# Performance work log

Measured on AMD Instinct MI355X. Metric: run time of the kernel, lower is better.

## Reference

```python
import jax, jax.numpy as jnp
import numpy as np

N, E, D, H, ED = 10000, 160000, 512, 256, 16
EPS = 1e-5  # BatchNorm1d eps


def _cgconv(x, src, dst, edge_attr, Wf, bf, Ws, bs, gamma, beta, mean, var):
    # PyG CGConv: z = [x_i, x_j, e_ij]; m = sigmoid(lin_f(z)) * softplus(lin_s(z));
    # aggr='add' at target i; batch_norm (eval mode, running stats) then residual.
    z = jnp.concatenate([x[dst], x[src], edge_attr], axis=1)  # [E, 2D+ED]
    m = jax.nn.sigmoid(z @ Wf + bf) * jax.nn.softplus(z @ Ws + bs)  # [E, D]
    aggr = jax.ops.segment_sum(m, dst, num_segments=x.shape[0])  # [N, D]
    bn = (aggr - mean) * jax.lax.rsqrt(var + EPS) * gamma + beta
    return x + bn


def _gcnconv(x, src, dst, W, b):
    # PyG GCNConv with add_self_loops=True, normalize=True:
    n = x.shape[0]
    deg = jax.ops.segment_sum(jnp.ones((src.shape[0],), x.dtype), dst, num_segments=n) + 1.0
    dinv = jax.lax.rsqrt(deg)  # [N]
    h = x @ W  # [N, out]
    out = jax.ops.segment_sum((dinv[src] * dinv[dst])[:, None] * h[src], dst, num_segments=n)
    out = out + (dinv * dinv)[:, None] * h  # self-loop contribution
    return out + b


def _forward(x, edge_attr, goal_feat,
             cg1_Wf, cg1_bf, cg1_Ws, cg1_bs, cg1_gamma, cg1_beta, cg1_mean, cg1_var,
             cg2_Wf, cg2_bf, cg2_Ws, cg2_bs, cg2_gamma, cg2_beta, cg2_mean, cg2_var,
             gcn3_W, gcn3_b, gcn4_W, gcn4_b, d1_W, d1_b, d2_W, d2_b, src, dst):
    # dropout layers are identity in eval mode (self.training=False)
    x = jax.nn.relu(_cgconv(x, src, dst, edge_attr, cg1_Wf, cg1_bf, cg1_Ws, cg1_bs,
                            cg1_gamma, cg1_beta, cg1_mean, cg1_var))
    x = jax.nn.relu(_cgconv(x, src, dst, edge_attr, cg2_Wf, cg2_bf, cg2_Ws, cg2_bs,
                            cg2_gamma, cg2_beta, cg2_mean, cg2_var))
    x = jax.nn.relu(_gcnconv(x, src, dst, gcn3_W, gcn3_b))
    x = jax.nn.relu(_gcnconv(x, src, dst, gcn4_W, gcn4_b))
    g = jnp.broadcast_to(goal_feat, (x.shape[0], goal_feat.shape[1]))  # repeat(num_nodes, 1)
    h = jax.nn.relu(jnp.concatenate([x, g], axis=1) @ d1_W + d1_b)
    return h @ d2_W + d2_b  # [N, 1]


def setup_inputs() -> dict:
    ks = jax.random.split(jax.random.key(0), 12)
    w = lambda k, s: jax.random.normal(k, s, dtype=jnp.float32) * 0.02
    Z = 2 * D + ED
    return {
        "x": jax.random.normal(ks[0], (N, D), jnp.float32),
        "edge_attr": jax.random.normal(ks[1], (E, ED), jnp.float32),
        "goal_feat": jax.random.normal(ks[2], (1, D), jnp.float32),
        "cg1_Wf": w(ks[3], (Z, D)), "cg1_bf": jnp.zeros((D,), jnp.float32),
        "cg1_Ws": w(ks[4], (Z, D)), "cg1_bs": jnp.zeros((D,), jnp.float32),
        "cg1_gamma": jnp.ones((D,), jnp.float32), "cg1_beta": jnp.zeros((D,), jnp.float32),
        "cg1_mean": jnp.zeros((D,), jnp.float32), "cg1_var": jnp.ones((D,), jnp.float32),
        "cg2_Wf": w(ks[5], (Z, D)), "cg2_bf": jnp.zeros((D,), jnp.float32),
        "cg2_Ws": w(ks[6], (Z, D)), "cg2_bs": jnp.zeros((D,), jnp.float32),
        "cg2_gamma": jnp.ones((D,), jnp.float32), "cg2_beta": jnp.zeros((D,), jnp.float32),
        "cg2_mean": jnp.zeros((D,), jnp.float32), "cg2_var": jnp.ones((D,), jnp.float32),
        "gcn3_W": w(ks[7], (D, H)), "gcn3_b": jnp.zeros((H,), jnp.float32),
        "gcn4_W": w(ks[8], (H, H)), "gcn4_b": jnp.zeros((H,), jnp.float32),
        "d1_W": w(ks[9], (H + D, D)), "d1_b": jnp.zeros((D,), jnp.float32),
        "d2_W": w(ks[10], (D, 1)), "d2_b": jnp.zeros((1,), jnp.float32),
        "edge_index": jax.random.randint(ks[11], (2, E), 0, N, dtype=jnp.int32),
        "batch": jnp.zeros((N,), jnp.int32),
    }


def reference(x, edge_attr, goal_feat,
              cg1_Wf, cg1_bf, cg1_Ws, cg1_bs, cg1_gamma, cg1_beta, cg1_mean, cg1_var,
              cg2_Wf, cg2_bf, cg2_Ws, cg2_bs, cg2_gamma, cg2_beta, cg2_mean, cg2_var,
              gcn3_W, gcn3_b, gcn4_W, gcn4_b, d1_W, d1_b, d2_W, d2_b,
              edge_index, batch):
    src, dst = edge_index[0], edge_index[1]
    return _forward(x, edge_attr, goal_feat,
                    cg1_Wf, cg1_bf, cg1_Ws, cg1_bs, cg1_gamma, cg1_beta, cg1_mean, cg1_var,
                    cg2_Wf, cg2_bf, cg2_Ws, cg2_bs, cg2_gamma, cg2_beta, cg2_mean, cg2_var,
                    gcn3_W, gcn3_b, gcn4_W, gcn4_b, d1_W, d1_b, d2_W, d2_b, src, dst)
```

## Files before the change

### kernel.cpp

```cpp
#include <hip/hip_runtime.h>
#include <math.h>

#define N_NODES 10000
#define N_EDGES 160000
#define DIM 512
#define HDIM 256
#define EDIM 16
#define BN_EPS 1e-5f
#define L2E 1.4426950408889634f
#define LN2 0.6931471805599453f

typedef unsigned short ushort_t;
typedef unsigned int uint_t;
typedef __attribute__((ext_vector_type(8))) short bf16x8;
typedef __attribute__((ext_vector_type(4))) float f32x4;
typedef __attribute__((ext_vector_type(2))) _Float16 half2_t;

__device__ __forceinline__ ushort_t f2bf(float x) {
    uint_t u = __float_as_uint(x);
    uint_t r = (u + 0x7FFF + ((u >> 16) & 1)) >> 16;
    return (ushort_t)r;
}
__device__ __forceinline__ float bf2f(ushort_t h) {
    return __uint_as_float(((uint_t)h) << 16);
}
__device__ __forceinline__ float bflo(uint_t u) {
    return __uint_as_float(u << 16);
}
__device__ __forceinline__ float bfhi(uint_t u) {
    return __uint_as_float(u & 0xffff0000u);
}
__device__ __forceinline__ void gld16(const void* g, void* l) {
    __builtin_amdgcn_global_load_lds(
        (const __attribute__((address_space(1))) unsigned int*)g,
        (__attribute__((address_space(3))) unsigned int*)l, 16, 0, 0);
}
__device__ __forceinline__ half2_t u2h(uint_t u) {
    return __builtin_bit_cast(half2_t, u);
}
__device__ __forceinline__ uint_t pk_f16(float a, float b) {
    return __builtin_bit_cast(uint_t, __builtin_amdgcn_cvt_pkrtz(a, b));
}
__device__ __forceinline__ float fexp2(float x) {
#if __has_builtin(__builtin_amdgcn_exp2f)
    return __builtin_amdgcn_exp2f(x);
#else
    return __expf(x * LN2);
#endif
}
__device__ __forceinline__ float flog2(float x) {
#if __has_builtin(__builtin_amdgcn_logf)
    return __builtin_amdgcn_logf(x);
#else
    return __logf(x) * L2E;
#endif
}
__device__ __forceinline__ void swz(int lid, int gx, int gy, int& bx, int& by) {
    int per = gy * 8;
    int grp = lid / per;
    int rem = lid - grp * per;
    int gsz = min(8, gx - grp * 8);
    by = rem / gsz;
    bx = grp * 8 + (rem - by * gsz);
}

__global__ void k_hist(const int* __restrict__ dst, int* __restrict__ cnt) {
    int e = blockIdx.x * blockDim.x + threadIdx.x;
    if (e < N_EDGES) atomicAdd(&cnt[dst[e]], 1);
}

__global__ __launch_bounds__(1024) void k_scan(int* __restrict__ offs, float* __restrict__ dinv) {
    __shared__ int wsum[16];
    int t = threadIdx.x, lane = t & 63, wv = t >> 6;
    int base_i = t * 10;
    int v[10];
    int s = 0;
#pragma unroll
    for (int k = 0; k < 10; k++) {
        int idx = base_i + k;
        int x = (idx < N_NODES) ? offs[idx] : 0;
        v[k] = x;
        s += x;
        if (idx < N_NODES) dinv[idx] = rsqrtf((float)x + 1.0f);
    }
    int ps = s;
#pragma unroll
    for (int off = 1; off < 64; off <<= 1) {
        int u = __shfl_up(ps, off, 64);
        if (lane >= off) ps += u;
    }
    if (lane == 63) wsum[wv] = ps;
    __syncthreads();
    if (wv == 0) {
        int w = (lane < 16) ? wsum[lane] : 0;
#pragma unroll
        for (int off = 1; off < 16; off <<= 1) {
            int u = __shfl_up(w, off, 64);
            if (lane >= off) w += u;
        }
        if (lane < 16) wsum[lane] = w;
    }
    __syncthreads();
    int wbase = (wv == 0) ? 0 : wsum[wv - 1];
    int run = wbase + ps - s;
#pragma unroll
    for (int k = 0; k < 10; k++) {
        int idx = base_i + k;
        if (idx < N_NODES) offs[idx] = run;
        run += v[k];
    }
    if (t == 1023) offs[N_NODES] = wsum[15];
}

__global__ void k_scatter(const int* __restrict__ srcv, const int* __restrict__ dstv,
                          const float* __restrict__ ea,
                          const int* __restrict__ offs, const float* __restrict__ dinv,
                          int* __restrict__ cursor,
                          int* __restrict__ srcQ, int* __restrict__ srcH,
                          float* __restrict__ dinvArr,
                          uint_t* __restrict__ eaP) {
    int e = blockIdx.x * blockDim.x + threadIdx.x;
    if (e >= N_EDGES) return;
    int d = dstv[e];
    int p = offs[d] + atomicAdd(&cursor[d], 1);
    int s = srcv[e];
    srcQ[p] = s << 11;
    srcH[p] = s << 9;
    dinvArr[p] = dinv[s];
    const float* er = ea + (size_t)e * EDIM;
    uint_t pk[8];
#pragma unroll
    for (int k2 = 0; k2 < 8; k2++) pk[k2] = pk_f16(er[2 * k2], er[2 * k2 + 1]);
    uint_t* q = eaP + (size_t)p * 8;
    *(uint4*)q = *(uint4*)&pk[0];
    *(uint4*)(q + 4) = *(uint4*)&pk[4];
}

__global__ __launch_bounds__(256) void k_cvtW(
    const float* __restrict__ Wf0, const float* __restrict__ Ws0,
    const float* __restrict__ Wf1, const float* __restrict__ Ws1,
    const float* __restrict__ g3W, const float* __restrict__ g4W,
    const float* __restrict__ d1W,
    ushort_t* __restrict__ W2cg0, ushort_t* __restrict__ W2cg1,
    ushort_t* __restrict__ W2g3, ushort_t* __restrict__ W2g4,
    ushort_t* __restrict__ W2d1)
{
    __shared__ ushort_t tle[64][72];
    int b = blockIdx.x, t = threadIdx.x;
    const float* src; int ldw, kin0, cin0, ldk, cout0, kout0; ushort_t* out; float scale;
    if (b < 512) {
        int layer = b >> 8, tt = b & 255;
        int g = tt >> 6, rem = tt & 63;
        int ct = rem >> 3, kt = rem & 7;
        const float* Wf = layer ? Wf1 : Wf0;
        const float* Ws = layer ? Ws1 : Ws0;
        src = (g & 1) ? Ws : Wf;
        ldw = 512; kin0 = ((g & 2) ? 512 : 0) + kt * 64; cin0 = ct * 64;
        out = layer ? W2cg1 : W2cg0; ldk = 512;
        cout0 = g * 512 + ct * 64; kout0 = kt * 64;
        scale = L2E;
    } else if (b < 544) {
        int tt = b - 512; int ct = tt >> 3, kt = tt & 7;
        src = g3W; ldw = 256; kin0 = kt * 64; cin0 = ct * 64;
        out = W2g3; ldk = 512; cout0 = ct * 64; kout0 = kt * 64; scale = 1.f;
    } else if (b < 560) {
        int tt = b - 544; int ct = tt >> 2, kt = tt & 3;
        src = g4W; ldw = 256; kin0 = kt * 64; cin0 = ct * 64;
        out = W2g4; ldk = 256; cout0 = ct * 64; kout0 = kt * 64; scale = 1.f;
    } else {
        int tt = b - 560; int ct = tt >> 2, kt = tt & 3;
        src = d1W; ldw = 512; kin0 = kt * 64; cin0 = ct * 64;
        out = W2d1; ldk = 256; cout0 = ct * 64; kout0 = kt * 64; scale = 1.f;
    }
    int c = t & 63;
    int k4 = t >> 6;
#pragma unroll
    for (int i = 0; i < 16; i++) {
        int k = k4 * 16 + i;
        tle[k][c] = f2bf(src[(size_t)(kin0 + k) * ldw + cin0 + c] * scale);
    }
    __syncthreads();
    int cl = t >> 2, kq = t & 3;
    ushort_t tmp[16];
#pragma unroll
    for (int j = 0; j < 16; j++) tmp[j] = tle[kq * 16 + j][cl];
    ushort_t* dst = out + (size_t)(cout0 + cl) * ldk + kout0 + kq * 16;
    *(uint4*)dst = *(uint4*)&tmp[0];
    *(uint4*)(dst + 8) = *(uint4*)&tmp[8];
}

#define MP_WEP   32
#define MP_GV    40
#define MP_END   20040

__global__ __launch_bounds__(256) void k_megaprep(
    const float* __restrict__ x, const float* __restrict__ goal,
    const float* __restrict__ Wf0, const float* __restrict__ Ws0,
    const float* __restrict__ Wf1, const float* __restrict__ Ws1,
    const float* __restrict__ d1W, const float* __restrict__ d1b,
    ushort_t* __restrict__ A2, uint_t* __restrict__ WEP, float* __restrict__ cgv)
{
    int b = blockIdx.x, t = threadIdx.x;
    if (b < MP_WEP) {
        int layer = b >> 4, blk = b & 15;
        int idx = blk * 256 + t;
        int c = idx >> 3, k2 = idx & 7;
        const float* Wf = (layer ? Wf1 : Wf0) + 1024 * 512;
        const float* Ws = (layer ? Ws1 : Ws0) + 1024 * 512;
        uint_t* WEPf = WEP + layer * 8192;
        uint_t* WEPs = WEPf + 4096;
        WEPf[c * 8 + k2] = pk_f16(Wf[(2 * k2) * 512 + c] * L2E, Wf[(2 * k2 + 1) * 512 + c] * L2E);
        WEPs[c * 8 + k2] = pk_f16(Ws[(2 * k2) * 512 + c] * L2E, Ws[(2 * k2 + 1) * 512 + c] * L2E);
    } else if (b < MP_GV) {
        __shared__ float red[256];
        int bb = b - MP_WEP;
        int c = bb * 64 + (t & 63);
        int slice = t >> 6;
        float acc = 0.f;
        for (int i = 0; i < 128; i++) {
            int k = slice * 128 + i;
            acc += goal[k] * d1W[(size_t)(256 + k) * 512 + c];
        }
        red[t] = acc;
        __syncthreads();
        if (t < 128) red[t] += red[t + 128];
        __syncthreads();
        if (t < 64) cgv[c] = red[t] + red[t + 64] + d1b[c];
    } else {
        int idx = (b - MP_GV) * 256 + t;
        if (idx < N_NODES * 512) A2[idx] = f2bf(x[idx]);
    }
}

__global__ __launch_bounds__(256) void k_gemm3(
    const ushort_t* __restrict__ A2, int K, int M,
    const ushort_t* __restrict__ W2t,
    float* __restrict__ outF, ushort_t* __restrict__ outQ,
    const float* __restrict__ bias, int mode, int ldc, int gx, int gy)
{
    __shared__ ushort_t As[128 * 64];
    __shared__ ushort_t Bs[128 * 64];
    int tid = threadIdx.x;
    int lane = tid & 63, w = tid >> 6;
    int wm = w & 1, wn = w >> 1;
    int lrow = lane & 15, quad = lane >> 4;
    int bx, by;
    swz(blockIdx.x, gx, gy, bx, by);
    int row0 = bx * 128, col0 = by * 128;

    f32x4 acc[4][4] = {};

    const ushort_t* ArG[4]; ushort_t* ArL[4];
    const ushort_t* BrG[4]; ushort_t* BrL[4];
#pragma unroll
    for (int p = 0; p < 4; p++) {
        int s = tid + 256 * p;
        int r = s >> 3, k8p = s & 7;
        int k8l = k8p ^ (r & 7);
        int gra = row0 + r; if (gra >= M) gra = M - 1;
        ArG[p] = A2 + (size_t)gra * K + k8l * 8;
        ArL[p] = As + s * 8;
        BrG[p] = W2t + (size_t)(col0 + r) * K + k8l * 8;
        BrL[p] = Bs + s * 8;
    }
    const ushort_t* afp[2][4];
    const ushort_t* bfp[2][4];
#pragma unroll
    for (int sl = 0; sl < 2; sl++)
#pragma unroll
        for (int mt = 0; mt < 4; mt++) {
            int r = wm * 64 + mt * 16 + lrow;
            afp[sl][mt] = As + (r * 8 + ((sl * 4 + quad) ^ (r & 7))) * 8;
            int c = wn * 64 + mt * 16 + lrow;
            bfp[sl][mt] = Bs + (c * 8 + ((sl * 4 + quad) ^ (c & 7))) * 8;
        }

    for (int k0 = 0; k0 < K; k0 += 64) {
        __syncthreads();
#pragma unroll
        for (int p = 0; p < 4; p++) {
            gld16(ArG[p] + k0, ArL[p]);
            gld16(BrG[p] + k0, BrL[p]);
        }
        __syncthreads();
#pragma unroll
        for (int sl = 0; sl < 2; sl++) {
            bf16x8 af[4], bff[4];
#pragma unroll
            for (int i = 0; i < 4; i++) {
                af[i]  = *(const bf16x8*)afp[sl][i];
                bff[i] = *(const bf16x8*)bfp[sl][i];
            }
#pragma unroll
            for (int mt = 0; mt < 4; mt++)
#pragma unroll
                for (int nt = 0; nt < 4; nt++)
                    acc[mt][nt] = __builtin_amdgcn_mfma_f32_16x16x32_bf16(
                        af[mt], bff[nt], acc[mt][nt], 0, 0, 0);
        }
    }

#pragma unroll
    for (int mt = 0; mt < 4; mt++) {
#pragma unroll
        for (int nt = 0; nt < 4; nt++) {
            int gcol = col0 + wn * 64 + nt * 16 + lrow;
#pragma unroll
            for (int r = 0; r < 4; r++) {
                int grow = row0 + wm * 64 + mt * 16 + quad * 4 + r;
                if (grow >= M) continue;
                float v = acc[mt][nt][r];
                if (mode == 1) {
                    if (gcol < 1024) {
                        outF[(size_t)grow * 1024 + gcol] = v;
                    } else {
                        int c = gcol - 1024;
                        int grp = c >> 9, cc = c & 511;
                        int pos = (cc >> 1) * 4 + grp * 2 + (cc & 1);
                        outQ[(size_t)grow * 1024 + pos] = f2bf(v);
                    }
                } else if (mode == 2) {
                    outF[(size_t)grow * ldc + gcol] = fmaxf(v + bias[gcol], 0.f);
                } else {
                    outQ[(size_t)grow * ldc + gcol] = f2bf(v);
                }
            }
        }
    }
}

__global__ __launch_bounds__(256) void k_gemm64(
    const ushort_t* __restrict__ A2, int K, int M,
    const ushort_t* __restrict__ W2t,
    float* __restrict__ outF, ushort_t* __restrict__ outQ,
    const float* __restrict__ bias, int mode, int ldc, int gx, int gy)
{
    __shared__ ushort_t As[64 * 64];
    __shared__ ushort_t Bs[128 * 64];
    int tid = threadIdx.x;
    int lane = tid & 63, w = tid >> 6;
    int lrow = lane & 15, quad = lane >> 4;
    int bx, by;
    swz(blockIdx.x, gx, gy, bx, by);
    int row0 = bx * 64, col0 = by * 128;

    f32x4 acc[4][2] = {};

    const ushort_t* ArG[2]; ushort_t* ArL[2];
    const ushort_t* BrG[4]; ushort_t* BrL[4];
#pragma unroll
    for (int p = 0; p < 2; p++) {
        int s = tid + 256 * p;
        int r = s >> 3, k8p = s & 7;
        int k8l = k8p ^ (r & 7);
        int gra = row0 + r; if (gra >= M) gra = M - 1;
        ArG[p] = A2 + (size_t)gra * K + k8l * 8;
        ArL[p] = As + s * 8;
    }
#pragma unroll
    for (int p = 0; p < 4; p++) {
        int s = tid + 256 * p;
        int r = s >> 3, k8p = s & 7;
        int k8l = k8p ^ (r & 7);
        BrG[p] = W2t + (size_t)(col0 + r) * K + k8l * 8;
        BrL[p] = Bs + s * 8;
    }
    const ushort_t* afp[2][4];
    const ushort_t* bfp[2][2];
#pragma unroll
    for (int sl = 0; sl < 2; sl++) {
#pragma unroll
        for (int mt = 0; mt < 4; mt++) {
            int r = mt * 16 + lrow;
            afp[sl][mt] = As + (r * 8 + ((sl * 4 + quad) ^ (r & 7))) * 8;
        }
#pragma unroll
        for (int nt = 0; nt < 2; nt++) {
            int c = w * 32 + nt * 16 + lrow;
            bfp[sl][nt] = Bs + (c * 8 + ((sl * 4 + quad) ^ (c & 7))) * 8;
        }
    }

    for (int k0 = 0; k0 < K; k0 += 64) {
        __syncthreads();
        gld16(ArG[0] + k0, ArL[0]);
        gld16(ArG[1] + k0, ArL[1]);
#pragma unroll
        for (int p = 0; p < 4; p++) gld16(BrG[p] + k0, BrL[p]);
        __syncthreads();
#pragma unroll
        for (int sl = 0; sl < 2; sl++) {
            bf16x8 af[4], bff[2];
#pragma unroll
            for (int i = 0; i < 4; i++) af[i] = *(const bf16x8*)afp[sl][i];
#pragma unroll
            for (int i = 0; i < 2; i++) bff[i] = *(const bf16x8*)bfp[sl][i];
#pragma unroll
            for (int mt = 0; mt < 4; mt++)
#pragma unroll
                for (int nt = 0; nt < 2; nt++)
                    acc[mt][nt] = __builtin_amdgcn_mfma_f32_16x16x32_bf16(
                        af[mt], bff[nt], acc[mt][nt], 0, 0, 0);
        }
    }

#pragma unroll
    for (int mt = 0; mt < 4; mt++) {
#pragma unroll
        for (int nt = 0; nt < 2; nt++) {
            int gcol = col0 + w * 32 + nt * 16 + lrow;
#pragma unroll
            for (int r = 0; r < 4; r++) {
                int grow = row0 + mt * 16 + quad * 4 + r;
                if (grow >= M) continue;
                float v = acc[mt][nt][r];
                if (mode == 2) outF[(size_t)grow * ldc + gcol] = fmaxf(v + bias[gcol], 0.f);
                else outQ[(size_t)grow * ldc + gcol] = f2bf(v);
            }
        }
    }
}

#define CG_BODY(curq, jj) do {                                                     \
    uint4 eA = *(const uint4*)&sEaP[jj][0];                                        \
    uint4 eB = *(const uint4*)&sEaP[jj][4];                                        \
    float gf0 = pf.x + bflo((curq).x), gf1 = pf.y + bfhi((curq).x);                \
    float gs0 = ps.x + bflo((curq).y), gs1 = ps.y + bfhi((curq).y);                \
    uint_t ek[8] = {eA.x, eA.y, eA.z, eA.w, eB.x, eB.y, eB.z, eB.w};               \
    _Pragma("unroll")                                                              \
    for (int k = 0; k < 8; k++) {                                                  \
        half2_t e2 = u2h(ek[k]);                                                   \
        gf0 = __builtin_amdgcn_fdot2(e2, u2h(wfp[0][k]), gf0, false);              \
        gf1 = __builtin_amdgcn_fdot2(e2, u2h(wfp[1][k]), gf1, false);              \
        gs0 = __builtin_amdgcn_fdot2(e2, u2h(wsp[0][k]), gs0, false);              \
        gs1 = __builtin_amdgcn_fdot2(e2, u2h(wsp[1][k]), gs1, false);              \
    }                                                                              \
    float sg0 = __builtin_amdgcn_rcpf(1.f + fexp2(-gf0));                          \
    float sg1 = __builtin_amdgcn_rcpf(1.f + fexp2(-gf1));                          \
    float sp0 = fmaxf(gs0, 0.f) + flog2(1.f + fexp2(-fabsf(gs0)));                 \
    float sp1 = fmaxf(gs1, 0.f) + flog2(1.f + fexp2(-fabsf(gs1)));                 \
    acc0 = fmaf(sg0, sp0, acc0);                                                   \
    acc1 = fmaf(sg1, sp1, acc1);                                                   \
} while (0)

__global__ __launch_bounds__(256) void k_cg_aggr(
    const float* __restrict__ xin, const float* __restrict__ P,
    const ushort_t* __restrict__ Qi,
    const uint_t* __restrict__ WEPf, const uint_t* __restrict__ WEPs,
    const float* __restrict__ bfv, const float* __restrict__ bsv,
    const float* __restrict__ gamma, const float* __restrict__ beta,
    const float* __restrict__ mean, const float* __restrict__ var,
    const int* __restrict__ offs, const int* __restrict__ srcQ,
    const uint_t* __restrict__ eaP,
    float* __restrict__ xout, ushort_t* __restrict__ A2out)
{
    int i = blockIdx.x;
    int t = threadIdx.x;
    int c0 = 2 * t;
    uint_t wfp[2][8], wsp[2][8];
    {
        const uint_t* pf8 = WEPf + c0 * 8;
        const uint_t* ps8 = WEPs + c0 * 8;
        *(uint4*)&wfp[0][0] = *(const uint4*)(pf8 + 0);
        *(uint4*)&wfp[0][4] = *(const uint4*)(pf8 + 4);
        *(uint4*)&wfp[1][0] = *(const uint4*)(pf8 + 8);
        *(uint4*)&wfp[1][4] = *(const uint4*)(pf8 + 12);
        *(uint4*)&wsp[0][0] = *(const uint4*)(ps8 + 0);
        *(uint4*)&wsp[0][4] = *(const uint4*)(ps8 + 4);
        *(uint4*)&wsp[1][0] = *(const uint4*)(ps8 + 8);
        *(uint4*)&wsp[1][4] = *(const uint4*)(ps8 + 12);
    }
    float2 pf = *(const float2*)&P[(size_t)i * 1024 + c0];
    float2 ps = *(const float2*)&P[(size_t)i * 1024 + 512 + c0];
    float2 bf2 = *(const float2*)&bfv[c0];
    float2 bs2 = *(const float2*)&bsv[c0];
    pf.x = fmaf(bf2.x, L2E, pf.x); pf.y = fmaf(bf2.y, L2E, pf.y);
    ps.x = fmaf(bs2.x, L2E, ps.x); ps.y = fmaf(bs2.y, L2E, ps.y);
    float acc0 = 0.f, acc1 = 0.f;
    int e0 = offs[i], e1 = offs[i + 1];
    __shared__ uint_t sEaP[32][8];
    __shared__ int sOff[36];
    const char* Qb = (const char*)(Qi + 4 * t);
    for (int base = e0; base < e1; base += 32) {
        int g = min(32, e1 - base);
        __syncthreads();
        if (t < 36) sOff[t] = (t < g) ? srcQ[base + t] : 0;
        {
            int j = t >> 3, k2 = t & 7;
            if (j < g) sEaP[j][k2] = eaP[(size_t)(base + j) * 8 + k2];
        }
        __syncthreads();
        uint2 q[4];
#pragma unroll
        for (int p = 0; p < 4; p++) q[p] = *(const uint2*)(Qb + (uint_t)sOff[p]);
        int j = 0;
        for (; j + 4 <= g; j += 4) {
#pragma unroll
            for (int u = 0; u < 4; u++) {
                uint2 cur = q[u];
                q[u] = *(const uint2*)(Qb + (uint_t)sOff[j + u + 4]);
                CG_BODY(cur, j + u);
            }
        }
#pragma unroll
        for (int u = 0; u < 3; u++) {
            if (j + u < g) CG_BODY(q[u], j + u);
        }
    }
    acc0 *= LN2;
    acc1 *= LN2;
    size_t ib = (size_t)i * DIM;
    float2 mn = *(const float2*)&mean[c0];
    float2 vr = *(const float2*)&var[c0];
    float2 gm = *(const float2*)&gamma[c0];
    float2 bt = *(const float2*)&beta[c0];
    float2 xi = *(const float2*)&xin[ib + c0];
    float bn0 = (acc0 - mn.x) * rsqrtf(vr.x + BN_EPS) * gm.x + bt.x;
    float bn1 = (acc1 - mn.y) * rsqrtf(vr.y + BN_EPS) * gm.y + bt.y;
    float o0 = fmaxf(xi.x + bn0, 0.f);
    float o1 = fmaxf(xi.y + bn1, 0.f);
    if (xout) *(float2*)&xout[ib + c0] = make_float2(o0, o1);
    ushort_t h0 = f2bf(o0), h1 = f2bf(o1);
    *(uint_t*)(A2out + (size_t)i * 512 + c0) = (uint_t)h0 | ((uint_t)h1 << 16);
}

__global__ __launch_bounds__(128) void k_gcn_aggr(
    const ushort_t* __restrict__ h, const float* __restrict__ dinv,
    const float* __restrict__ bias,
    const int* __restrict__ offs, const int* __restrict__ srcH,
    const float* __restrict__ dinvArr, ushort_t* __restrict__ A2out)
{
    int i = blockIdx.x;
    int t = threadIdx.x;
    int c0 = 2 * t;
    float acc0 = 0.f, acc1 = 0.f;
    int e0 = offs[i], e1 = offs[i + 1];
    __shared__ int sS[40];
    __shared__ float sD[40];
    const char* hb = (const char*)(h + c0);
    for (int base = e0; base < e1; base += 32) {
        int g = min(32, e1 - base);
        __syncthreads();
        if (t < 40) {
            bool ok = (t < g);
            sS[t] = ok ? srcH[base + t] : 0;
            sD[t] = ok ? dinvArr[base + t] : 0.f;
        }
        __syncthreads();
        uint_t q[8];
#pragma unroll
        for (int p = 0; p < 8; p++) q[p] = *(const uint_t*)(hb + (uint_t)sS[p]);
        int j = 0;
        for (; j + 8 <= g; j += 8) {
#pragma unroll
            for (int u = 0; u < 8; u++) {
                uint_t cur = q[u];
                q[u] = *(const uint_t*)(hb + (uint_t)sS[j + u + 8]);
                float d = sD[j + u];
                acc0 = fmaf(d, bflo(cur), acc0);
                acc1 = fmaf(d, bfhi(cur), acc1);
            }
        }
#pragma unroll
        for (int u = 0; u < 7; u++) {
            if (j + u < g) {
                uint_t cur = q[u];
                float d = sD[j + u];
                acc0 = fmaf(d, bflo(cur), acc0);
                acc1 = fmaf(d, bfhi(cur), acc1);
            }
        }
    }
    float di = dinv[i];
    uint_t qi = *(const uint_t*)(h + (size_t)i * HDIM + c0);
    float2 b2 = *(const float2*)&bias[c0];
    float o0 = fmaxf(di * acc0 + di * di * bflo(qi) + b2.x, 0.f);
    float o1 = fmaxf(di * acc1 + di * di * bfhi(qi) + b2.y, 0.f);
    ushort_t h0 = f2bf(o0), h1 = f2bf(o1);
    *(uint_t*)(A2out + (size_t)i * 256 + c0) = (uint_t)h0 | ((uint_t)h1 << 16);
}

__global__ __launch_bounds__(256) void k_final(const float* __restrict__ hd,
                                               const float* __restrict__ w2,
                                               const float* __restrict__ b2,
                                               float* __restrict__ out) {
    int wave = threadIdx.x >> 6, lane = threadIdx.x & 63;
    int i = blockIdx.x * 4 + wave;
    if (i >= N_NODES) return;
    const float* r = hd + (size_t)i * DIM;
    float acc = 0.f;
#pragma unroll
    for (int q = 0; q < 8; q++) acc += r[lane + 64 * q] * w2[lane + 64 * q];
#pragma unroll
    for (int off = 32; off > 0; off >>= 1) acc += __shfl_down(acc, off, 64);
    if (lane == 0) out[i] = acc + b2[0];
}

extern "C" void kernel_launch(void* const* d_in, const int* in_sizes, int n_in,
                              void* d_out, int out_size, void* d_ws, size_t ws_size,
                              hipStream_t stream) {
    (void)in_sizes; (void)n_in; (void)out_size; (void)ws_size;
    const float* x      = (const float*)d_in[0];
    const float* ea     = (const float*)d_in[1];
    const float* goal   = (const float*)d_in[2];
    const float* cgWf[2] = {(const float*)d_in[3],  (const float*)d_in[11]};
    const float* cgbf[2] = {(const float*)d_in[4],  (const float*)d_in[12]};
    const float* cgWs[2] = {(const float*)d_in[5],  (const float*)d_in[13]};
    const float* cgbs[2] = {(const float*)d_in[6],  (const float*)d_in[14]};
    const float* cggm[2] = {(const float*)d_in[7],  (const float*)d_in[15]};
    const float* cgbt[2] = {(const float*)d_in[8],  (const float*)d_in[16]};
    const float* cgmn[2] = {(const float*)d_in[9],  (const float*)d_in[17]};
    const float* cgvr[2] = {(const float*)d_in[10], (const float*)d_in[18]};
    const float* gcn3_W = (const float*)d_in[19];
    const float* gcn3_b = (const float*)d_in[20];
    const float* gcn4_W = (const float*)d_in[21];
    const float* gcn4_b = (const float*)d_in[22];
    const float* d1_W   = (const float*)d_in[23];
    const float* d1_b   = (const float*)d_in[24];
    const float* d2_W   = (const float*)d_in[25];
    const float* d2_b   = (const float*)d_in[26];
    const int*   eidx   = (const int*)d_in[27];
    const int*   srcv   = eidx;
    const int*   dstv   = eidx + N_EDGES;
    float* outp = (float*)d_out;

    char* w = (char*)d_ws;
    float*    Pbuf  = (float*)w;                      w += (size_t)N_NODES * 1024 * 4;
    ushort_t* Qbuf  = (ushort_t*)w;                   w += (size_t)N_NODES * 1024 * 2;
    float*    xB    = (float*)w;                      w += (size_t)N_NODES * 512 * 4;
    ushort_t* A2    = (ushort_t*)w;                   w += (size_t)N_NODES * 512 * 2;
    ushort_t* A3    = (ushort_t*)w;                   w += (size_t)N_NODES * 256 * 2;
    ushort_t* W2cg0 = (ushort_t*)w;                   w += (size_t)2048 * 512 * 2;
    ushort_t* W2cg1 = (ushort_t*)w;                   w += (size_t)2048 * 512 * 2;
    ushort_t* W2g3  = (ushort_t*)w;                   w += (size_t)256 * 512 * 2;
    ushort_t* W2g4  = (ushort_t*)w;                   w += (size_t)256 * 256 * 2;
    ushort_t* W2d1  = (ushort_t*)w;                   w += (size_t)512 * 256 * 2;
    uint_t*   eaP   = (uint_t*)w;                     w += (size_t)N_EDGES * 8 * 4;
    uint_t*   WEP   = (uint_t*)w;                     w += 16384 * 4;
    float*    cgv   = (float*)w;                      w += 512 * 4;
    int*      srcQ    = (int*)w;                      w += N_EDGES * 4;
    int*      srcH    = (int*)w;                      w += N_EDGES * 4;
    float*    dinvArr = (float*)w;                    w += N_EDGES * 4;
    int*      offs    = (int*)w;                      w += (N_NODES + 1) * 4;
    int*      cursor  = (int*)w;                      w += N_NODES * 4;
    float*    dinv    = (float*)w;                    w += N_NODES * 4;
    uint_t* WEPf[2] = {WEP, WEP + 8192};
    uint_t* WEPs[2] = {WEP + 4096, WEP + 12288};
    ushort_t* h3 = (ushort_t*)Pbuf;
    float*    hd = (float*)Qbuf;

    k_cvtW<<<592, 256, 0, stream>>>(cgWf[0], cgWs[0], cgWf[1], cgWs[1],
                                    gcn3_W, gcn4_W, d1_W,
                                    W2cg0, W2cg1, W2g3, W2g4, W2d1);
    k_megaprep<<<MP_END, 256, 0, stream>>>(x, goal,
        cgWf[0], cgWs[0], cgWf[1], cgWs[1], d1_W, d1_b, A2, WEP, cgv);

    hipMemsetAsync(offs, 0, (N_NODES + 1) * sizeof(int), stream);
    hipMemsetAsync(cursor, 0, N_NODES * sizeof(int), stream);
    k_hist<<<(N_EDGES + 255) / 256, 256, 0, stream>>>(dstv, offs);
    k_scan<<<1, 1024, 0, stream>>>(offs, dinv);
    k_scatter<<<(N_EDGES + 255) / 256, 256, 0, stream>>>(srcv, dstv, ea, offs, dinv,
                                                         cursor, srcQ, srcH, dinvArr, eaP);

    k_gemm3<<<79 * 16, 256, 0, stream>>>(A2, 512, N_NODES, W2cg0,
                                         Pbuf, Qbuf, nullptr, 1, 0, 79, 16);
    k_cg_aggr<<<N_NODES, 256, 0, stream>>>(x, Pbuf, Qbuf, WEPf[0], WEPs[0],
                                           cgbf[0], cgbs[0],
                                           cggm[0], cgbt[0], cgmn[0], cgvr[0],
                                           offs, srcQ, eaP, xB, A2);
    k_gemm3<<<79 * 16, 256, 0, stream>>>(A2, 512, N_NODES, W2cg1,
                                         Pbuf, Qbuf, nullptr, 1, 0, 79, 16);
    k_cg_aggr<<<N_NODES, 256, 0, stream>>>(xB, Pbuf, Qbuf, WEPf[1], WEPs[1],
                                           cgbf[1], cgbs[1],
                                           cggm[1], cgbt[1], cgmn[1], cgvr[1],
                                           offs, srcQ, eaP, nullptr, A2);

    k_gemm64<<<157 * 2, 256, 0, stream>>>(A2, 512, N_NODES, W2g3,
                                          nullptr, h3, nullptr, 3, HDIM, 157, 2);
    k_gcn_aggr<<<N_NODES, 128, 0, stream>>>(h3, dinv, gcn3_b, offs, srcH, dinvArr, A3);

    k_gemm64<<<157 * 2, 256, 0, stream>>>(A3, 256, N_NODES, W2g4,
                                          nullptr, h3, nullptr, 3, HDIM, 157, 2);
    k_gcn_aggr<<<N_NODES, 128, 0, stream>>>(h3, dinv, gcn4_b, offs, srcH, dinvArr, A3);

    k_gemm64<<<157 * 4, 256, 0, stream>>>(A3, 256, N_NODES, W2d1,
                                          hd, nullptr, cgv, 2, DIM, 157, 4);
    k_final<<<(N_NODES + 3) / 4, 256, 0, stream>>>(hd, d2_W, d2_b, outp);
}
```

Measured before the change: 536.0 us.

## Compute CGConv edge-feature projection with MFMA and stage neighbor rows in LDS

Rewrites the CGConv aggregation kernel so the per-edge edge_attr projection (16-dim) runs on 16x16x16 f16 MFMA instructions instead of per-thread fdot2 loops. Neighbor Q rows for 16 edges at a time are gathered into shared memory with coalesced 16-byte loads, and the results are reduced across lanes with shuffles. Biases are folded into the P GEMM epilogue, and the BatchNorm scale and shift are precomputed by a new small prep kernel. The cost is a larger LDS footprint (about 37 KB per block), padded batches of 16 edges, and extra syncs and shuffle reductions.

```diff
diff --git a/kernel.cpp b/kernel.cpp
--- a/kernel.cpp
+++ b/kernel.cpp
@@ -15,15 +15,14 @@
 typedef __attribute__((ext_vector_type(8))) short bf16x8;
 typedef __attribute__((ext_vector_type(4))) float f32x4;
 typedef __attribute__((ext_vector_type(2))) _Float16 half2_t;
+typedef __attribute__((ext_vector_type(4))) _Float16 f16x4;
+typedef __attribute__((ext_vector_type(2))) unsigned int u32x2;
 
 __device__ __forceinline__ ushort_t f2bf(float x) {
     uint_t u = __float_as_uint(x);
     uint_t r = (u + 0x7FFF + ((u >> 16) & 1)) >> 16;
     return (ushort_t)r;
 }
-__device__ __forceinline__ float bf2f(ushort_t h) {
-    return __uint_as_float(((uint_t)h) << 16);
-}
 __device__ __forceinline__ float bflo(uint_t u) {
     return __uint_as_float(u << 16);
 }
@@ -34,9 +33,6 @@
     __builtin_amdgcn_global_load_lds(
         (const __attribute__((address_space(1))) unsigned int*)g,
         (__attribute__((address_space(3))) unsigned int*)l, 16, 0, 0);
-}
-__device__ __forceinline__ half2_t u2h(uint_t u) {
-    return __builtin_bit_cast(half2_t, u);
 }
 __device__ __forceinline__ uint_t pk_f16(float a, float b) {
     return __builtin_bit_cast(uint_t, __builtin_amdgcn_cvt_pkrtz(a, b));
@@ -189,6 +185,32 @@
     *(uint4*)(dst + 8) = *(uint4*)&tmp[8];
 }
 
+__global__ __launch_bounds__(256) void k_prep2(
+    const float* __restrict__ bf0, const float* __restrict__ bs0,
+    const float* __restrict__ gm0, const float* __restrict__ bt0,
+    const float* __restrict__ mn0, const float* __restrict__ vr0,
+    const float* __restrict__ bf1, const float* __restrict__ bs1,
+    const float* __restrict__ gm1, const float* __restrict__ bt1,
+    const float* __restrict__ mn1, const float* __restrict__ vr1,
+    float* __restrict__ biasCG, float* __restrict__ bnS, float* __restrict__ bnB)
+{
+    int layer = blockIdx.x;
+    const float* bf = layer ? bf1 : bf0;
+    const float* bs = layer ? bs1 : bs0;
+    const float* gm = layer ? gm1 : gm0;
+    const float* bt = layer ? bt1 : bt0;
+    const float* mn = layer ? mn1 : mn0;
+    const float* vr = layer ? vr1 : vr0;
+    int t = threadIdx.x;
+    for (int c = t; c < 512; c += 256) {
+        biasCG[layer * 1024 + c] = bf[c] * L2E;
+        biasCG[layer * 1024 + 512 + c] = bs[c] * L2E;
+        float rs = rsqrtf(vr[c] + BN_EPS) * gm[c];
+        bnS[layer * 512 + c] = LN2 * rs;
+        bnB[layer * 512 + c] = bt[c] - mn[c] * rs;
+    }
+}
+
 #define MP_WEP   32
 #define MP_GV    40
 #define MP_END   20040
@@ -198,19 +220,21 @@
     const float* __restrict__ Wf0, const float* __restrict__ Ws0,
     const float* __restrict__ Wf1, const float* __restrict__ Ws1,
     const float* __restrict__ d1W, const float* __restrict__ d1b,
-    ushort_t* __restrict__ A2, uint_t* __restrict__ WEP, float* __restrict__ cgv)
+    ushort_t* __restrict__ A2, uint_t* __restrict__ WB, float* __restrict__ cgv)
 {
     int b = blockIdx.x, t = threadIdx.x;
     if (b < MP_WEP) {
-        int layer = b >> 4, blk = b & 15;
-        int idx = blk * 256 + t;
-        int c = idx >> 3, k2 = idx & 7;
-        const float* Wf = (layer ? Wf1 : Wf0) + 1024 * 512;
-        const float* Ws = (layer ? Ws1 : Ws0) + 1024 * 512;
-        uint_t* WEPf = WEP + layer * 8192;
-        uint_t* WEPs = WEPf + 4096;
-        WEPf[c * 8 + k2] = pk_f16(Wf[(2 * k2) * 512 + c] * L2E, Wf[(2 * k2 + 1) * 512 + c] * L2E);
-        WEPs[c * 8 + k2] = pk_f16(Ws[(2 * k2) * 512 + c] * L2E, Ws[(2 * k2 + 1) * 512 + c] * L2E);
+        int layer = b >> 4;
+        int tt = (b & 15) * 256 + t;
+        int tile = tt >> 6, ln = tt & 63;
+        int m = ln & 15, kq = ln >> 4;
+        const float* Wsrc = (tile < 32) ? (layer ? Wf1 : Wf0) : (layer ? Ws1 : Ws0);
+        int col = ((tile < 32) ? tile : tile - 32) * 16 + m;
+        const float* wr = Wsrc + (size_t)(1024 + kq * 4) * 512 + col;
+        uint_t u0 = pk_f16(wr[0] * L2E, wr[512] * L2E);
+        uint_t u1 = pk_f16(wr[1024] * L2E, wr[1536] * L2E);
+        uint_t* o = WB + (size_t)layer * 8192 + (size_t)tt * 2;
+        o[0] = u0; o[1] = u1;
     } else if (b < MP_GV) {
         __shared__ float red[256];
         int bb = b - MP_WEP;
@@ -312,12 +336,9 @@
                 float v = acc[mt][nt][r];
                 if (mode == 1) {
                     if (gcol < 1024) {
-                        outF[(size_t)grow * 1024 + gcol] = v;
+                        outF[(size_t)grow * 1024 + gcol] = v + bias[gcol];
                     } else {
-                        int c = gcol - 1024;
-                        int grp = c >> 9, cc = c & 511;
-                        int pos = (cc >> 1) * 4 + grp * 2 + (cc & 1);
-                        outQ[(size_t)grow * 1024 + pos] = f2bf(v);
+                        outQ[(size_t)grow * 1024 + gcol - 1024] = f2bf(v);
                     }
                 } else if (mode == 2) {
                     outF[(size_t)grow * ldc + gcol] = fmaxf(v + bias[gcol], 0.f);
@@ -421,107 +442,112 @@
     }
 }
 
-#define CG_BODY(curq, jj) do {                                                     \
-    uint4 eA = *(const uint4*)&sEaP[jj][0];                                        \
-    uint4 eB = *(const uint4*)&sEaP[jj][4];                                        \
-    float gf0 = pf.x + bflo((curq).x), gf1 = pf.y + bfhi((curq).x);                \
-    float gs0 = ps.x + bflo((curq).y), gs1 = ps.y + bfhi((curq).y);                \
-    uint_t ek[8] = {eA.x, eA.y, eA.z, eA.w, eB.x, eB.y, eB.z, eB.w};               \
-    _Pragma("unroll")                                                              \
-    for (int k = 0; k < 8; k++) {                                                  \
-        half2_t e2 = u2h(ek[k]);                                                   \
-        gf0 = __builtin_amdgcn_fdot2(e2, u2h(wfp[0][k]), gf0, false);              \
-        gf1 = __builtin_amdgcn_fdot2(e2, u2h(wfp[1][k]), gf1, false);              \
-        gs0 = __builtin_amdgcn_fdot2(e2, u2h(wsp[0][k]), gs0, false);              \
-        gs1 = __builtin_amdgcn_fdot2(e2, u2h(wsp[1][k]), gs1, false);              \
-    }                                                                              \
-    float sg0 = __builtin_amdgcn_rcpf(1.f + fexp2(-gf0));                          \
-    float sg1 = __builtin_amdgcn_rcpf(1.f + fexp2(-gf1));                          \
-    float sp0 = fmaxf(gs0, 0.f) + flog2(1.f + fexp2(-fabsf(gs0)));                 \
-    float sp1 = fmaxf(gs1, 0.f) + flog2(1.f + fexp2(-fabsf(gs1)));                 \
-    acc0 = fmaf(sg0, sp0, acc0);                                                   \
-    acc1 = fmaf(sg1, sp1, acc1);                                                   \
-} while (0)
+#define QROWB 2064
 
 __global__ __launch_bounds__(256) void k_cg_aggr(
     const float* __restrict__ xin, const float* __restrict__ P,
     const ushort_t* __restrict__ Qi,
-    const uint_t* __restrict__ WEPf, const uint_t* __restrict__ WEPs,
-    const float* __restrict__ bfv, const float* __restrict__ bsv,
-    const float* __restrict__ gamma, const float* __restrict__ beta,
-    const float* __restrict__ mean, const float* __restrict__ var,
+    const uint_t* __restrict__ WB,
+    const float* __restrict__ bnS, const float* __restrict__ bnB,
     const int* __restrict__ offs, const int* __restrict__ srcQ,
     const uint_t* __restrict__ eaP,
     float* __restrict__ xout, ushort_t* __restrict__ A2out)
 {
+    __shared__ char sQ[16 * QROWB];
+    __shared__ float sP[1024];
+    __shared__ int sOff[16];
     int i = blockIdx.x;
     int t = threadIdx.x;
+    int lane = t & 63, w = t >> 6;
+    int es = lane & 15;
+    int qsel = lane >> 4;
+
+    f16x4 wbF[8], wbS[8];
+#pragma unroll
+    for (int j = 0; j < 8; j++) {
+        int pt = w * 8 + j;
+        wbF[j] = __builtin_bit_cast(f16x4, *(const u32x2*)&WB[(size_t)pt * 128 + lane * 2]);
+        wbS[j] = __builtin_bit_cast(f16x4, *(const u32x2*)&WB[(size_t)(32 + pt) * 128 + lane * 2]);
+    }
+    *(float4*)&sP[t * 4] = *(const float4*)&P[(size_t)i * 1024 + t * 4];
+
+    int e0 = offs[i], e1 = offs[i + 1];
+    f32x4 acc[8] = {};
+    const char* Qb = (const char*)Qi;
+    const char* ebg = (const char*)eaP;
+    int qoff8 = qsel * 8;
+
+    for (int base = e0; base < e1; base += 16) {
+        int g = min(16, e1 - base);
+        __syncthreads();
+        if (t < 16) sOff[t] = srcQ[min(base + t, e1 - 1)];
+        __syncthreads();
+#pragma unroll
+        for (int it = 0; it < 8; it++) {
+            int gi = it * 256 + t;
+            int e = gi >> 7, c = gi & 127;
+            uint4 d = *(const uint4*)(Qb + (uint_t)sOff[e] + c * 16);
+            if (e >= g) d = make_uint4(0xFF80FF80u, 0xFF80FF80u, 0xFF80FF80u, 0xFF80FF80u);
+            *(uint4*)(sQ + e * QROWB + c * 16) = d;
+        }
+        int ce = min(base + es, e1 - 1);
+        f16x4 efr = __builtin_bit_cast(f16x4, *(const u32x2*)(ebg + (size_t)ce * 32 + qoff8));
+        __syncthreads();
+        const char* qrow = sQ + es * QROWB + qoff8;
+#pragma unroll
+        for (int j = 0; j < 8; j++) {
+            int pt = w * 8 + j;
+            u32x2 qf = *(const u32x2*)(qrow + pt * 32);
+            u32x2 qs = *(const u32x2*)(qrow + 1024 + pt * 32);
+            f32x4 zero = {0.f, 0.f, 0.f, 0.f};
+            f32x4 df  = __builtin_amdgcn_mfma_f32_16x16x16f16(wbF[j], efr, zero, 0, 0, 0);
+            f32x4 dsv = __builtin_amdgcn_mfma_f32_16x16x16f16(wbS[j], efr, zero, 0, 0, 0);
+            f32x4 pf4 = *(const f32x4*)&sP[pt * 16 + qsel * 4];
+            f32x4 ps4 = *(const f32x4*)&sP[512 + pt * 16 + qsel * 4];
+            float qfv[4] = {bflo(qf.x), bfhi(qf.x), bflo(qf.y), bfhi(qf.y)};
+            float qsv[4] = {bflo(qs.x), bfhi(qs.x), bflo(qs.y), bfhi(qs.y)};
+#pragma unroll
+            for (int r = 0; r < 4; r++) {
+                float gf = df[r] + pf4[r] + qfv[r];
+                float gs = dsv[r] + ps4[r] + qsv[r];
+                float sg = __builtin_amdgcn_rcpf(1.f + fexp2(-gf));
+                float sp = fmaxf(gs, 0.f) + flog2(1.f + fexp2(-fabsf(gs)));
+                acc[j][r] = fmaf(sg, sp, acc[j][r]);
+            }
+        }
+    }
+
+#pragma unroll
+    for (int j = 0; j < 8; j++)
+#pragma unroll
+        for (int r = 0; r < 4; r++) {
+            float v = acc[j][r];
+            v += __shfl_xor(v, 1, 64);
+            v += __shfl_xor(v, 2, 64);
+            v += __shfl_xor(v, 4, 64);
+            v += __shfl_xor(v, 8, 64);
+            acc[j][r] = v;
+        }
+    __syncthreads();
+    float* sAcc = (float*)sQ;
+    if (es == 0) {
+#pragma unroll
+        for (int j = 0; j < 8; j++)
+#pragma unroll
+            for (int r = 0; r < 4; r++)
+                sAcc[(w * 8 + j) * 16 + qsel * 4 + r] = acc[j][r];
+    }
+    __syncthreads();
     int c0 = 2 * t;
-    uint_t wfp[2][8], wsp[2][8];
-    {
-        const uint_t* pf8 = WEPf + c0 * 8;
-        const uint_t* ps8 = WEPs + c0 * 8;
-        *(uint4*)&wfp[0][0] = *(const uint4*)(pf8 + 0);
-        *(uint4*)&wfp[0][4] = *(const uint4*)(pf8 + 4);
-        *(uint4*)&wfp[1][0] = *(const uint4*)(pf8 + 8);
-        *(uint4*)&wfp[1][4] = *(const uint4*)(pf8 + 12);
-        *(uint4*)&wsp[0][0] = *(const uint4*)(ps8 + 0);
-        *(uint4*)&wsp[0][4] = *(const uint4*)(ps8 + 4);
-        *(uint4*)&wsp[1][0] = *(const uint4*)(ps8 + 8);
-        *(uint4*)&wsp[1][4] = *(const uint4*)(ps8 + 12);
-    }
-    float2 pf = *(const float2*)&P[(size_t)i * 1024 + c0];
-    float2 ps = *(const float2*)&P[(size_t)i * 1024 + 512 + c0];
-    float2 bf2 = *(const float2*)&bfv[c0];
-    float2 bs2 = *(const float2*)&bsv[c0];
-    pf.x = fmaf(bf2.x, L2E, pf.x); pf.y = fmaf(bf2.y, L2E, pf.y);
-    ps.x = fmaf(bs2.x, L2E, ps.x); ps.y = fmaf(bs2.y, L2E, ps.y);
-    float acc0 = 0.f, acc1 = 0.f;
-    int e0 = offs[i], e1 = offs[i + 1];
-    __shared__ uint_t sEaP[32][8];
-    __shared__ int sOff[36];
-    const char* Qb = (const char*)(Qi + 4 * t);
-    for (int base = e0; base < e1; base += 32) {
-        int g = min(32, e1 - base);
-        __syncthreads();
-        if (t < 36) sOff[t] = (t < g) ? srcQ[base + t] : 0;
-        {
-            int j = t >> 3, k2 = t & 7;
-            if (j < g) sEaP[j][k2] = eaP[(size_t)(base + j) * 8 + k2];
-        }
-        __syncthreads();
-        uint2 q[4];
-#pragma unroll
-        for (int p = 0; p < 4; p++) q[p] = *(const uint2*)(Qb + (uint_t)sOff[p]);
-        int j = 0;
-        for (; j + 4 <= g; j += 4) {
-#pragma unroll
-            for (int u = 0; u < 4; u++) {
-                uint2 cur = q[u];
-                q[u] = *(const uint2*)(Qb + (uint_t)sOff[j + u + 4]);
-                CG_BODY(cur, j + u);
-            }
-        }
-#pragma unroll
-        for (int u = 0; u < 3; u++) {
-            if (j + u < g) CG_BODY(q[u], j + u);
-        }
-    }
-    acc0 *= LN2;
-    acc1 *= LN2;
+    float a0 = sAcc[c0], a1 = sAcc[c0 + 1];
+    float2 s2 = *(const float2*)&bnS[c0];
+    float2 b2 = *(const float2*)&bnB[c0];
     size_t ib = (size_t)i * DIM;
-    float2 mn = *(const float2*)&mean[c0];
-    float2 vr = *(const float2*)&var[c0];
-    float2 gm = *(const float2*)&gamma[c0];
-    float2 bt = *(const float2*)&beta[c0];
     float2 xi = *(const float2*)&xin[ib + c0];
-    float bn0 = (acc0 - mn.x) * rsqrtf(vr.x + BN_EPS) * gm.x + bt.x;
-    float bn1 = (acc1 - mn.y) * rsqrtf(vr.y + BN_EPS) * gm.y + bt.y;
-    float o0 = fmaxf(xi.x + bn0, 0.f);
-    float o1 = fmaxf(xi.y + bn1, 0.f);
+    float o0 = fmaxf(xi.x + fmaf(a0, s2.x, b2.x), 0.f);
+    float o1 = fmaxf(xi.y + fmaf(a1, s2.y, b2.y), 0.f);
     if (xout) *(float2*)&xout[ib + c0] = make_float2(o0, o1);
-    ushort_t h0 = f2bf(o0), h1 = f2bf(o1);
-    *(uint_t*)(A2out + (size_t)i * 512 + c0) = (uint_t)h0 | ((uint_t)h1 << 16);
+    *(uint_t*)(A2out + (size_t)i * 512 + c0) = (uint_t)f2bf(o0) | ((uint_t)f2bf(o1) << 16);
 }
 
 __global__ __launch_bounds__(128) void k_gcn_aggr(
@@ -636,24 +662,28 @@
     ushort_t* W2g4  = (ushort_t*)w;                   w += (size_t)256 * 256 * 2;
     ushort_t* W2d1  = (ushort_t*)w;                   w += (size_t)512 * 256 * 2;
     uint_t*   eaP   = (uint_t*)w;                     w += (size_t)N_EDGES * 8 * 4;
-    uint_t*   WEP   = (uint_t*)w;                     w += 16384 * 4;
+    uint_t*   WB    = (uint_t*)w;                     w += 16384 * 4;
     float*    cgv   = (float*)w;                      w += 512 * 4;
+    float*    biasCG = (float*)w;                     w += 2048 * 4;
+    float*    bnS    = (float*)w;                     w += 1024 * 4;
+    float*    bnB    = (float*)w;                     w += 1024 * 4;
     int*      srcQ    = (int*)w;                      w += N_EDGES * 4;
     int*      srcH    = (int*)w;                      w += N_EDGES * 4;
     float*    dinvArr = (float*)w;                    w += N_EDGES * 4;
     int*      offs    = (int*)w;                      w += (N_NODES + 1) * 4;
     int*      cursor  = (int*)w;                      w += N_NODES * 4;
     float*    dinv    = (float*)w;                    w += N_NODES * 4;
-    uint_t* WEPf[2] = {WEP, WEP + 8192};
-    uint_t* WEPs[2] = {WEP + 4096, WEP + 12288};
     ushort_t* h3 = (ushort_t*)Pbuf;
     float*    hd = (float*)Qbuf;
 
     k_cvtW<<<592, 256, 0, stream>>>(cgWf[0], cgWs[0], cgWf[1], cgWs[1],
                                     gcn3_W, gcn4_W, d1_W,
                                     W2cg0, W2cg1, W2g3, W2g4, W2d1);
+    k_prep2<<<2, 256, 0, stream>>>(cgbf[0], cgbs[0], cggm[0], cgbt[0], cgmn[0], cgvr[0],
+                                   cgbf[1], cgbs[1], cggm[1], cgbt[1], cgmn[1], cgvr[1],
+                                   biasCG, bnS, bnB);
     k_megaprep<<<MP_END, 256, 0, stream>>>(x, goal,
-        cgWf[0], cgWs[0], cgWf[1], cgWs[1], d1_W, d1_b, A2, WEP, cgv);
+        cgWf[0], cgWs[0], cgWf[1], cgWs[1], d1_W, d1_b, A2, WB, cgv);
 
     hipMemsetAsync(offs, 0, (N_NODES + 1) * sizeof(int), stream);
     hipMemsetAsync(cursor, 0, N_NODES * sizeof(int), stream);
@@ -663,17 +693,14 @@
                                                          cursor, srcQ, srcH, dinvArr, eaP);
 
     k_gemm3<<<79 * 16, 256, 0, stream>>>(A2, 512, N_NODES, W2cg0,
-                                         Pbuf, Qbuf, nullptr, 1, 0, 79, 16);
-    k_cg_aggr<<<N_NODES, 256, 0, stream>>>(x, Pbuf, Qbuf, WEPf[0], WEPs[0],
-                                           cgbf[0], cgbs[0],
-                                           cggm[0], cgbt[0], cgmn[0], cgvr[0],
-                                           offs, srcQ, eaP, xB, A2);
+                                         Pbuf, Qbuf, biasCG, 1, 0, 79, 16);
+    k_cg_aggr<<<N_NODES, 256, 0, stream>>>(x, Pbuf, Qbuf, WB,
+                                           bnS, bnB, offs, srcQ, eaP, xB, A2);
     k_gemm3<<<79 * 16, 256, 0, stream>>>(A2, 512, N_NODES, W2cg1,
-                                         Pbuf, Qbuf, nullptr, 1, 0, 79, 16);
-    k_cg_aggr<<<N_NODES, 256, 0, stream>>>(xB, Pbuf, Qbuf, WEPf[1], WEPs[1],
-                                           cgbf[1], cgbs[1],
-                                           cggm[1], cgbt[1], cgmn[1], cgvr[1],
-                                           offs, srcQ, eaP, nullptr, A2);
+                                         Pbuf, Qbuf, biasCG + 1024, 1, 0, 79, 16);
+    k_cg_aggr<<<N_NODES, 256, 0, stream>>>(xB, Pbuf, Qbuf, WB + 8192,
+                                           bnS + 512, bnB + 512, offs, srcQ, eaP,
+                                           nullptr, A2);
 
     k_gemm64<<<157 * 2, 256, 0, stream>>>(A2, 512, N_NODES, W2g3,
                                           nullptr, h3, nullptr, 3, HDIM, 157, 2);
```

Result: slower. 691.8 us (+29.1%).
